# Performance work log

Hardware: AMD Instinct MI355X
Metric: run time of the kernel (lower is better)

## Reference

```python
import jax, jax.numpy as jnp
import numpy as np

# Scattering2D hyperparameters (kymatio-style Morlet filter bank)
J, L, M, N = 2, 8, 224, 224
SIGMA0 = 0.8
XI0 = 3.0 * np.pi / 4.0
SLANT = 4.0 / L


def _fold(h, k):
    """Fourier-domain subsampling / filter periodization: fold and average k x k blocks."""
    if k == 1:
        return h
    Mh, Nh = h.shape[-2], h.shape[-1]
    return h.reshape(h.shape[:-2] + (k, Mh // k, k, Nh // k)).mean(axis=(-4, -2))


def _freq_grid():
    wx = (2 * np.pi * np.fft.fftfreq(M)).astype(np.float64)[:, None]
    wy = (2 * np.pi * np.fft.fftfreq(N)).astype(np.float64)[None, :]
    return wx, wy


def _morlet_hat(theta, xi, sigma):
    wx, wy = _freq_grid()
    u = np.cos(theta) * wx + np.sin(theta) * wy
    v = -np.sin(theta) * wx + np.cos(theta) * wy
    gab = np.exp(-0.5 * sigma ** 2 * ((u - xi) ** 2 + (v / SLANT) ** 2))
    gauss = np.exp(-0.5 * sigma ** 2 * (u ** 2 + (v / SLANT) ** 2))
    kappa = np.exp(-0.5 * sigma ** 2 * xi ** 2)  # zero-mean Morlet correction
    return (gab - kappa * gauss).astype(np.float32)


def _build_filters():
    psi = {}
    for j in range(J):
        f = np.stack([_morlet_hat(l * np.pi / L, XI0 / 2 ** j, SIGMA0 * 2 ** j) for l in range(L)])
        psi[j] = [_fold(f, 2 ** r) for r in range(j + 1)]  # periodized to each resolution
    wx, wy = _freq_grid()
    sig_phi = SIGMA0 * 2 ** (J - 1)
    phi0 = np.exp(-0.5 * sig_phi ** 2 * (wx ** 2 + wy ** 2)).astype(np.float32)
    phi = [_fold(phi0, 2 ** r) for r in range(J)]
    return psi, phi


PSI, PHI = _build_filters()


def _scattering(x):
    # x: (B, C, M, N) float32 -> (B, C, K, M/2^J, N/2^J), K = 1 + J*L + L^2*J*(J-1)/2
    xh = jnp.fft.fft2(x)
    s0 = jnp.fft.ifft2(_fold(xh * PHI[0], 2 ** J)).real[..., None, :, :]
    s1s, s2s = [], []
    for j1 in range(J):
        # first order: bandpass, subsample to resolution j1, modulus
        u1h = _fold(xh[..., None, :, :] * PSI[j1][0], 2 ** j1)       # (B,C,L,M/2^j1,N/2^j1)
        u1 = jnp.abs(jnp.fft.ifft2(u1h))
        u1h2 = jnp.fft.fft2(u1)
        s1s.append(jnp.fft.ifft2(_fold(u1h2 * PHI[j1], 2 ** (J - j1))).real)
        for j2 in range(j1 + 1, J):
            # second order over all (theta1, theta2) pairs, vectorized over L x L
            u2h = _fold(u1h2[..., None, :, :] * PSI[j2][j1], 2 ** (j2 - j1))  # (B,C,L,L,.,.)
            u2 = jnp.abs(jnp.fft.ifft2(u2h))
            s2 = jnp.fft.ifft2(_fold(jnp.fft.fft2(u2) * PHI[j2], 2 ** (J - j2))).real
            s2s.append(s2.reshape(s2.shape[:2] + (L * L,) + s2.shape[-2:]))
    return jnp.concatenate([s0] + s1s + s2s, axis=2)


def setup_inputs() -> dict:
    key = jax.random.key(0)
    k1, k2, _ = jax.random.split(key, 3)
    x = jax.random.normal(k1, (16, 3, M, N), dtype=jnp.float32)
    W_last = jax.random.normal(k2, (1000, 243), dtype=jnp.float32) * 0.02
    b_last = jnp.zeros((1000,), dtype=jnp.float32)
    return {"x": x, "W_last": W_last, "b_last": b_last}


def reference(x, W_last, b_last):
    s = _scattering(x)                                   # (B, 3, 81, 56, 56)
    B = s.shape[0]
    s = s.reshape(B, s.shape[1] * s.shape[2], s.shape[3], s.shape[4])  # flatten(1,2)
    g = s.max(axis=(-2, -1))                             # global max pool -> (B, 243)
    return g @ W_last.T + b_last                         # (B, 1000)
```

## Files before the change

kernel.cpp:

```cpp
#include <hip/hip_runtime.h>
#include <math.h>

#define PI_D 3.14159265358979323846
#define PI_F 3.14159265358979323846f

#define IMG224 50176
#define IMG112 12544
static const size_t OFF_FT224F = 0;
static const size_t OFF_FT224I = 2048;
static const size_t OFF_FT112F = 4096;
static const size_t OFF_FT112I = 6144;
static const size_t OFF_PHW    = 8600;
static const size_t OFF_PSI   = 257152;
static const size_t OFF_GK    = 1122688;
static const size_t OFF_XH    = 1126784;
static const size_t OFF_POOL  = 5943680;

__device__ inline unsigned fkey(float v) {
    int b = __float_as_int(v);
    return (b >= 0) ? ((unsigned)b | 0x80000000u) : ~(unsigned)b;
}
__device__ inline float funkey(unsigned u) {
    int b = (u & 0x80000000u) ? (int)(u & 0x7fffffffu) : (int)~u;
    return __int_as_float(b);
}
__device__ inline void cmac(float2& a, float2 z, float2 w) {
    a.x += z.x * w.x - z.y * w.y;
    a.y += z.x * w.y + z.y * w.x;
}
__device__ inline float2 cmulc(float2 v, float c, float s) {
    return make_float2(v.x * c - v.y * s, v.x * s + v.y * c);
}

struct C7 { float s; float wr[3][3]; float wi[3][3]; };
__device__ inline void ld7(const float2* __restrict__ W7, C7& c) {
    c.s = W7[0].x;
#pragma unroll
    for (int m = 1; m <= 3; ++m)
#pragma unroll
        for (int k = 1; k <= 3; ++k) {
            float2 w = W7[m * 7 + k];
            c.wr[m - 1][k - 1] = w.x;
            c.wi[m - 1][k - 1] = w.y;
        }
}
__device__ inline void dft7(const C7& c, const float2 t[7], float2 X[7]) {
    float2 a1 = make_float2(t[1].x + t[6].x, t[1].y + t[6].y);
    float2 b1 = make_float2(t[1].x - t[6].x, t[1].y - t[6].y);
    float2 a2 = make_float2(t[2].x + t[5].x, t[2].y + t[5].y);
    float2 b2 = make_float2(t[2].x - t[5].x, t[2].y - t[5].y);
    float2 a3 = make_float2(t[3].x + t[4].x, t[3].y + t[4].y);
    float2 b3 = make_float2(t[3].x - t[4].x, t[3].y - t[4].y);
    float bx = c.s * t[0].x, by = c.s * t[0].y;
    X[0] = make_float2(c.s * (t[0].x + a1.x + a2.x + a3.x),
                       c.s * (t[0].y + a1.y + a2.y + a3.y));
#pragma unroll
    for (int k = 0; k < 3; ++k) {
        float Px = c.wr[0][k] * a1.x + c.wr[1][k] * a2.x + c.wr[2][k] * a3.x;
        float Py = c.wr[0][k] * a1.y + c.wr[1][k] * a2.y + c.wr[2][k] * a3.y;
        float Qx = c.wi[0][k] * b1.x + c.wi[1][k] * b2.x + c.wi[2][k] * b3.x;
        float Qy = c.wi[0][k] * b1.y + c.wi[1][k] * b2.y + c.wi[2][k] * b3.y;
        X[k + 1] = make_float2(bx + Px - Qy, by + Py + Qx);
        X[6 - k] = make_float2(bx + Px + Qy, by + Py - Qx);
    }
}

template<int SGN>
__device__ inline void fft16(float2* x) {
    const float C8  = 0.70710678118654752f;
    const float C16 = 0.92387953251128674f;
    const float S16 = 0.38268343236508977f;
    const float sg = (float)SGN;
    float2 g[16];
#pragma unroll
    for (int b = 0; b < 4; ++b) {
        float2 x0 = x[b], x1 = x[4 + b], x2 = x[8 + b], x3 = x[12 + b];
        float2 e0 = make_float2(x0.x + x2.x, x0.y + x2.y);
        float2 e1 = make_float2(x0.x - x2.x, x0.y - x2.y);
        float2 o0 = make_float2(x1.x + x3.x, x1.y + x3.y);
        float2 o1 = make_float2(x1.x - x3.x, x1.y - x3.y);
        float2 io1 = (SGN > 0) ? make_float2(-o1.y, o1.x) : make_float2(o1.y, -o1.x);
        g[b * 4 + 0] = make_float2(e0.x + o0.x, e0.y + o0.y);
        g[b * 4 + 2] = make_float2(e0.x - o0.x, e0.y - o0.y);
        g[b * 4 + 1] = make_float2(e1.x + io1.x, e1.y + io1.y);
        g[b * 4 + 3] = make_float2(e1.x - io1.x, e1.y - io1.y);
    }
    g[5]  = cmulc(g[5],  C16,  sg * S16);
    g[6]  = cmulc(g[6],  C8,   sg * C8);
    g[7]  = cmulc(g[7],  S16,  sg * C16);
    g[9]  = cmulc(g[9],  C8,   sg * C8);
    g[10] = (SGN > 0) ? make_float2(-g[10].y, g[10].x)
                      : make_float2(g[10].y, -g[10].x);
    g[11] = cmulc(g[11], -C8,  sg * C8);
    g[13] = cmulc(g[13], S16,  sg * C16);
    g[14] = cmulc(g[14], -C8,  sg * C8);
    g[15] = cmulc(g[15], -C16, -sg * S16);
#pragma unroll
    for (int p = 0; p < 4; ++p) {
        float2 x0 = g[p], x1 = g[4 + p], x2 = g[8 + p], x3 = g[12 + p];
        float2 e0 = make_float2(x0.x + x2.x, x0.y + x2.y);
        float2 e1 = make_float2(x0.x - x2.x, x0.y - x2.y);
        float2 o0 = make_float2(x1.x + x3.x, x1.y + x3.y);
        float2 o1 = make_float2(x1.x - x3.x, x1.y - x3.y);
        float2 io1 = (SGN > 0) ? make_float2(-o1.y, o1.x) : make_float2(o1.y, -o1.x);
        x[p + 0]  = make_float2(e0.x + o0.x, e0.y + o0.y);
        x[p + 8]  = make_float2(e0.x - o0.x, e0.y - o0.y);
        x[p + 4]  = make_float2(e1.x + io1.x, e1.y + io1.y);
        x[p + 12] = make_float2(e1.x - io1.x, e1.y - io1.y);
    }
}

__global__ void k_fact(float2* o, int N1, int N2, double sign, double scale, int r2) {
    int base3 = N1 * N1 + N2 * N2 + N2 * N1;
    int total = base3 + (r2 ? 63 : 0);
    int N = N1 * N2;
    for (int i = blockIdx.x * blockDim.x + threadIdx.x; i < total; i += blockDim.x * gridDim.x) {
        double ang; double sc = 1.0;
        if (i < N1 * N1) {
            int n1 = i / N1, k1 = i % N1;
            ang = sign * 2.0 * PI_D * (double)((n1 * k1) % N1) / (double)N1;
        } else if (i < N1 * N1 + N2 * N2) {
            int j = i - N1 * N1; int n2 = j / N2, k2 = j % N2;
            ang = sign * 2.0 * PI_D * (double)((n2 * k2) % N2) / (double)N2;
            sc = scale;
        } else if (i < base3) {
            int j = i - N1 * N1 - N2 * N2; int n2 = j / N1, k1 = j % N1;
            ang = sign * 2.0 * PI_D * (double)((n2 * k1) % N) / (double)N;
        } else if (i < base3 + 49) {
            int j = i - base3; int n = j / 7, k = j % 7;
            ang = sign * 2.0 * PI_D * (double)((n * k) % 7) / 7.0;
            sc = scale;
        } else {
            int k = i - base3 - 49;
            ang = sign * 2.0 * PI_D * (double)k / 14.0;
        }
        o[i] = make_float2((float)(sc * cos(ang)), (float)(sc * sin(ang)));
    }
}

__global__ void k_psi(float* out) {
    int i = blockIdx.x * blockDim.x + threadIdx.x;
    if (i >= 16 * IMG224) return;
    int jl = i / IMG224, p = i % IMG224;
    int r = p / 224, c = p % 224;
    int j = jl >> 3, l = jl & 7;
    float fr = (r < 112) ? (float)r : (float)(r - 224);
    float fc = (c < 112) ? (float)c : (float)(c - 224);
    float wx = 2.0f * PI_F * fr / 224.0f;
    float wy = 2.0f * PI_F * fc / 224.0f;
    float theta = (float)l * PI_F / 8.0f;
    float xi = (3.0f * PI_F / 4.0f) / (float)(1 << j);
    float sg = 0.8f * (float)(1 << j);
    float ct = cosf(theta), st = sinf(theta);
    float u = ct * wx + st * wy;
    float v = -st * wx + ct * wy;
    float vs = v * 2.0f;
    float s2 = 0.5f * sg * sg;
    float gab = expf(-s2 * ((u - xi) * (u - xi) + vs * vs));
    float gau = expf(-s2 * (u * u + vs * vs));
    float kap = expf(-s2 * xi * xi);
    out[i] = gab - kap * gau;
}

__global__ void k_zero(unsigned* gk, int n) {
    int i = blockIdx.x * blockDim.x + threadIdx.x;
    if (i < n) gk[i] = 0u;
}

template<int N1, int N2, int TA, int FOLD, int BS, int RMODE, int SGN>
__global__ __launch_bounds__(BS) void rk(
    const void* __restrict__ inBase, int inShift,
    const float* __restrict__ fltBase, int fltMask,
    const float2* __restrict__ FT, float2* __restrict__ out,
    int swzImg, int inStride, int inOff)
{
    constexpr int N = N1 * N2;
    constexpr int NIN = N * FOLD;
    constexpr int ZS = N + 2;
    constexpr int TS = N2 * (N1 + 1);
    constexpr int K1H = N1 / 2;
    constexpr int TAC = (RMODE == 2) ? TA / 2 : TA;
    __shared__ float2 Z[TA * ZS];
    __shared__ float2 T[TA * TS];
    const float2* TW = FT + N1 * N1 + N2 * N2;
    const int bx = blockIdx.x, a0 = blockIdx.y * TA, t = threadIdx.x;
    int gIn, gFlt, gOut;
    if (swzImg > 0) {
        int img = bx % swzImg, sub = bx / swzImg;
        gIn = img * inStride + inOff + (sub >> 3);
        gFlt = sub & fltMask;
        gOut = img * (gridDim.x / swzImg) + sub;
    } else if (swzImg < 0) {
        int lgF = -swzImg;
        int xcd = bx & 7, loc = bx >> 3;
        int img = xcd * ((int)gridDim.x >> (3 + lgF)) + (loc >> lgF);
        int f = loc & ((1 << lgF) - 1);
        gIn = img; gFlt = f & fltMask; gOut = (img << lgF) + f;
    } else {
        gIn = bx >> inShift; gFlt = bx & fltMask; gOut = bx;
    }

    if (RMODE == 1) {
        const float* in = (const float*)inBase + (size_t)gIn * N * N;
#pragma unroll
        for (int r = 0; r < TA; ++r)
            for (int b = t; b < N; b += BS)
                Z[r * ZS + b] = make_float2(in[(size_t)(a0 + r) * N + b], 0.f);
    } else if (RMODE == 2) {
        const float* in = (const float*)inBase + (size_t)gIn * N * N;
#pragma unroll
        for (int pr = 0; pr < TAC; ++pr)
            for (int b = t; b < N; b += BS) {
                size_t base = (size_t)(a0 + 2 * pr) * N + b;
                Z[pr * ZS + b] = make_float2(in[base], in[base + N]);
            }
    } else {
        const float2* in = (const float2*)inBase + (size_t)gIn * (NIN * NIN);
        const float* flt = fltBase + (size_t)gFlt * (NIN * NIN);
        const float s = 1.0f / (float)(FOLD * FOLD);
#pragma unroll
        for (int r = 0; r < TA; ++r) {
            int a = a0 + r;
            for (int b = t; b < N; b += BS) {
                float re = 0.f, im = 0.f;
#pragma unroll
                for (int i = 0; i < FOLD; ++i)
#pragma unroll
                    for (int j = 0; j < FOLD; ++j) {
                        int idx = (a + N * i) * NIN + (b + N * j);
                        float2 v = in[idx];
                        float f = flt[idx];
                        re += v.x * f; im += v.y * f;
                    }
                Z[r * ZS + b] = make_float2(re * s, im * s);
            }
        }
    }
    __syncthreads();
    for (int idx = t; idx < TAC * N2 * 2; idx += BS) {
        int r = idx / (N2 * 2);
        int rem = idx % (N2 * 2);
        int n2 = rem / 2, h = rem % 2;
        float2 xx[N1];
#pragma unroll
        for (int n1 = 0; n1 < N1; ++n1) xx[n1] = Z[r * ZS + n1 * N2 + n2];
        fft16<SGN>(xx);
#pragma unroll
        for (int kk = 0; kk < K1H; ++kk) {
            int k1 = h * K1H + kk;
            float2 tw = TW[n2 * N1 + k1];
            T[r * TS + n2 * (N1 + 1) + k1] = cmulc(xx[k1], tw.x, tw.y);
        }
    }
    __syncthreads();
    {
        const float2* W7  = FT + N1 * N1 + N2 * N2 + N2 * N1;
        const float2* T14 = W7 + 49;
        for (int idx = t; idx < TAC * N1; idx += BS) {
            int r = idx / N1, k1 = idx % N1;
            float2 E[7], O[7];
#pragma unroll
            for (int k = 0; k < 7; ++k) { E[k] = make_float2(0.f, 0.f); O[k] = make_float2(0.f, 0.f); }
            for (int m = 0; m < 7; ++m) {
                float2 te = T[r * TS + (2 * m) * (N1 + 1) + k1];
                float2 to = T[r * TS + (2 * m + 1) * (N1 + 1) + k1];
#pragma unroll
                for (int k = 0; k < 7; ++k) {
                    float2 w = W7[m * 7 + k];
                    cmac(E[k], te, w);
                    cmac(O[k], to, w);
                }
            }
#pragma unroll
            for (int k = 0; k < 14; ++k) {
                float2 tw = T14[k];
                float2 o_ = O[k % 7];
                float2 X = E[k % 7];
                X.x += o_.x * tw.x - o_.y * tw.y;
                X.y += o_.x * tw.y + o_.y * tw.x;
                Z[r * ZS + k1 + N1 * k] = X;
            }
        }
    }
    __syncthreads();
    if (RMODE == 2) {
#pragma unroll
        for (int pr = 0; pr < TAC; ++pr) {
            float2* oe = out + ((size_t)gOut * N + (a0 + 2 * pr)) * N;
            float2* oo = oe + N;
            for (int b = t; b < N; b += BS) {
                int mb = (b == 0) ? 0 : N - b;
                float2 zk = Z[pr * ZS + b];
                float2 zm = Z[pr * ZS + mb];
                oe[b] = make_float2(0.5f * (zk.x + zm.x), 0.5f * (zk.y - zm.y));
                oo[b] = make_float2(0.5f * (zk.y + zm.y), 0.5f * (zm.x - zk.x));
            }
        }
    } else {
#pragma unroll
        for (int r = 0; r < TA; ++r) {
            float2* o = out + ((size_t)gOut * N + (a0 + r)) * N;
            for (int b = t; b < N; b += BS) o[b] = Z[r * ZS + b];
        }
    }
}

template<int N1, int N2, int SPLIT, int BS, int SGN>
__global__ __launch_bounds__(BS) void ck1(
    const float2* __restrict__ in, const float2* __restrict__ FT, float2* __restrict__ out)
{
    constexpr int N = N1 * N2;
    constexpr int NC = N / SPLIT;
    const float2* TW = FT + N1 * N1 + N2 * N2;
    const int g = blockIdx.x / SPLIT, half = blockIdx.x % SPLIT;
    const int n2 = blockIdx.y, t = threadIdx.x;
    if (2 * t >= NC) return;
    const int b0 = 2 * t + half * NC;
    const float2* I = in + (size_t)g * N * N;
    float2 a0[16], a1[16];
#pragma unroll
    for (int n1 = 0; n1 < 16; ++n1) {
        float4 v = *reinterpret_cast<const float4*>(&I[(size_t)(n1 * N2 + n2) * N + b0]);
        a0[n1] = make_float2(v.x, v.y);
        a1[n1] = make_float2(v.z, v.w);
    }
    fft16<SGN>(a0);
    fft16<SGN>(a1);
#pragma unroll
    for (int k1 = 0; k1 < 16; ++k1) {
        float2 tw = TW[n2 * N1 + k1];
        float2 r0 = cmulc(a0[k1], tw.x, tw.y);
        float2 r1 = cmulc(a1[k1], tw.x, tw.y);
        *reinterpret_cast<float4*>(&out[((size_t)g * N + (k1 * N2 + n2)) * N + b0]) =
            make_float4(r0.x, r0.y, r1.x, r1.y);
    }
}

template<int N1, int N2, int SPLIT, int MODE, int BS>
__global__ __launch_bounds__(BS) void ck2(
    const float2* __restrict__ in, const float2* __restrict__ FT,
    float2* __restrict__ outc, float* __restrict__ outr)
{
    constexpr int N = N1 * N2;
    constexpr int NC = N / SPLIT;
    const int g = blockIdx.x / SPLIT, half = blockIdx.x % SPLIT;
    const int k1 = blockIdx.y, t = threadIdx.x;
    if (2 * t >= NC) return;
    const int b0 = 2 * t + half * NC;
    const float2* I = in + (size_t)g * N * N;
    const float2* W7  = FT + N1 * N1 + N2 * N2 + N2 * N1;
    const float2* T14 = W7 + 49;
    float2 E0[7], E1[7], O0[7], O1[7];
#pragma unroll
    for (int k = 0; k < 7; ++k) {
        E0[k] = make_float2(0.f, 0.f); E1[k] = make_float2(0.f, 0.f);
        O0[k] = make_float2(0.f, 0.f); O1[k] = make_float2(0.f, 0.f);
    }
#pragma unroll
    for (int m = 0; m < 7; ++m) {
        float4 ve = *reinterpret_cast<const float4*>(&I[(size_t)(k1 * 14 + 2 * m) * N + b0]);
        float4 vo = *reinterpret_cast<const float4*>(&I[(size_t)(k1 * 14 + 2 * m + 1) * N + b0]);
        float2 ve0 = make_float2(ve.x, ve.y), ve1 = make_float2(ve.z, ve.w);
        float2 vo0 = make_float2(vo.x, vo.y), vo1 = make_float2(vo.z, vo.w);
#pragma unroll
        for (int k = 0; k < 7; ++k) {
            float2 w = W7[m * 7 + k];
            cmac(E0[k], ve0, w); cmac(E1[k], ve1, w);
            cmac(O0[k], vo0, w); cmac(O1[k], vo1, w);
        }
    }
#pragma unroll
    for (int k = 0; k < 14; ++k) {
        float2 tw = T14[k];
        float2 r0 = E0[k % 7], r1 = E1[k % 7];
        float2 o0 = O0[k % 7], o1 = O1[k % 7];
        r0.x += o0.x * tw.x - o0.y * tw.y;
        r0.y += o0.x * tw.y + o0.y * tw.x;
        r1.x += o1.x * tw.x - o1.y * tw.y;
        r1.y += o1.x * tw.y + o1.y * tw.x;
        if (MODE == 0) {
            *reinterpret_cast<float4*>(&outc[((size_t)g * N + (k1 + N1 * k)) * N + b0]) =
                make_float4(r0.x, r0.y, r1.x, r1.y);
        } else {
            size_t o = ((size_t)g * N + (k1 + N1 * k)) * N + b0;
            outr[o]     = sqrtf(r0.x * r0.x + r0.y * r0.y);
            outr[o + 1] = sqrtf(r1.x * r1.x + r1.y * r1.y);
        }
    }
}

template<int SGN, int BS, int EPI>
__device__ inline void fft112_2d(float2* Z, const float2* __restrict__ FT, int t)
{
    constexpr int ZS = 113;
    constexpr int NCH = (112 * 16 + BS - 1) / BS;
    const float2* W2 = FT + 256;
    const float2* TW = FT + 256 + 49;
    C7 c7; ld7(W2, c7);
    for (int idx = t; idx < 112 * 7; idx += BS) {
        int r = idx % 112, n2 = idx / 112;
        float2 xx[16];
#pragma unroll
        for (int n1 = 0; n1 < 16; ++n1) xx[n1] = Z[r * ZS + n1 * 7 + n2];
        fft16<SGN>(xx);
#pragma unroll
        for (int k1 = 0; k1 < 16; ++k1) {
            float2 tw = TW[n2 * 16 + k1];
            Z[r * ZS + k1 * 7 + n2] = cmulc(xx[k1], tw.x, tw.y);
        }
    }
    __syncthreads();
    {
        float2 tv[NCH][7];
#pragma unroll
        for (int c = 0; c < NCH; ++c) {
            int idx = c * BS + t;
            if (idx < 112 * 16) {
                int r = idx >> 4, k1 = idx & 15;
#pragma unroll
                for (int m = 0; m < 7; ++m) tv[c][m] = Z[r * ZS + k1 * 7 + m];
            }
        }
        __syncthreads();
#pragma unroll
        for (int c = 0; c < NCH; ++c) {
            int idx = c * BS + t;
            if (idx < 112 * 16) {
                int r = idx >> 4, k1 = idx & 15;
                float2 X[7];
                dft7(c7, tv[c], X);
#pragma unroll
                for (int k = 0; k < 7; ++k) Z[r * ZS + k1 + 16 * k] = X[k];
            }
        }
    }
    __syncthreads();
    for (int idx = t; idx < 112 * 7; idx += BS) {
        int b = idx % 112, n2 = idx / 112;
        float2 xx[16];
#pragma unroll
        for (int n1 = 0; n1 < 16; ++n1) xx[n1] = Z[(n1 * 7 + n2) * ZS + b];
        fft16<SGN>(xx);
#pragma unroll
        for (int k1 = 0; k1 < 16; ++k1) {
            float2 tw = TW[n2 * 16 + k1];
            Z[(k1 * 7 + n2) * ZS + b] = cmulc(xx[k1], tw.x, tw.y);
        }
    }
    __syncthreads();
    {
        float2 tv[NCH][7];
#pragma unroll
        for (int c = 0; c < NCH; ++c) {
            int idx = c * BS + t;
            if (idx < 112 * 16) {
                int b = idx >> 4, k1 = idx & 15;
#pragma unroll
                for (int m = 0; m < 7; ++m) tv[c][m] = Z[(k1 * 7 + m) * ZS + b];
            }
        }
        __syncthreads();
#pragma unroll
        for (int c = 0; c < NCH; ++c) {
            int idx = c * BS + t;
            if (idx < 112 * 16) {
                int b = idx >> 4, k1 = idx & 15;
                float2 X[7];
                dft7(c7, tv[c], X);
#pragma unroll
                for (int k = 0; k < 7; ++k) {
                    Z[(k1 + 16 * k) * ZS + b] =
                        EPI ? make_float2(sqrtf(X[k].x * X[k].x + X[k].y * X[k].y), 0.f)
                            : X[k];
                }
            }
        }
    }
    __syncthreads();
}

template<int BS>
__global__ __launch_bounds__(BS) void sc2pipe(
    const float2* __restrict__ inBase, const float* __restrict__ psiBase,
    const float* __restrict__ taps, const float2* __restrict__ FTI,
    unsigned* __restrict__ gk, int slotBase, int inStride, int subShift)
{
    constexpr int ZS = 113;
    __shared__ float2 Z[112 * ZS];
    __shared__ float2 F[56 * 57];
    __shared__ float red[BS / 64];
    const int t = threadIdx.x, bx = blockIdx.x;
    const int nimg = (int)gridDim.x >> subShift;
    const int xcd = bx & 7, local = bx >> 3;
    const int img = xcd * (nimg >> 3) + (local >> subShift);
    const int sub = local & ((1 << subShift) - 1);
    const float2* in = inBase + (size_t)(img * inStride + (sub >> 3)) * (224 * 224);
    const float* flt = psiBase + (size_t)(sub & 7) * (224 * 224);
    float gw[6];
#pragma unroll
    for (int i = 0; i < 6; ++i) gw[i] = taps[i];

    for (int idx = t; idx < 112 * 112; idx += BS) {
        int a = idx / 112, b = idx % 112;
        float re = 0.f, im = 0.f;
#pragma unroll
        for (int i = 0; i < 2; ++i)
#pragma unroll
            for (int j = 0; j < 2; ++j) {
                int p = (a + 112 * i) * 224 + (b + 112 * j);
                float2 v = in[p]; float f = flt[p];
                re += v.x * f; im += v.y * f;
            }
        Z[a * ZS + b] = make_float2(re * 0.25f, im * 0.25f);
    }
    __syncthreads();

    fft112_2d<1, BS, 1>(Z, FTI, t);

    float* Ft = (float*)F;
    for (int idx = t; idx < 112 * 56; idx += BS) {
        int r = idx % 112, cp = idx / 112;
        int c0 = 2 * cp;
        float acc = gw[0] * Z[r * ZS + c0].x;
#pragma unroll
        for (int m = 1; m <= 5; ++m) {
            int cm = c0 - m; cm += (cm < 0) ? 112 : 0;
            int cq = c0 + m; cq -= (cq >= 112) ? 112 : 0;
            acc += gw[m] * (Z[r * ZS + cm].x + Z[r * ZS + cq].x);
        }
        Ft[r * 57 + cp] = acc;
    }
    __syncthreads();

    float mx = -INFINITY;
    for (int idx = t; idx < 56 * 56; idx += BS) {
        int j = idx % 56, ip = idx / 56;
        int r0 = 2 * ip;
        float acc = gw[0] * Ft[r0 * 57 + j];
#pragma unroll
        for (int m = 1; m <= 5; ++m) {
            int ra = r0 - m; ra += (ra < 0) ? 112 : 0;
            int rb = r0 + m; rb -= (rb >= 112) ? 112 : 0;
            acc += gw[m] * (Ft[ra * 57 + j] + Ft[rb * 57 + j]);
        }
        mx = fmaxf(mx, acc);
    }
    for (int off = 32; off > 0; off >>= 1) mx = fmaxf(mx, __shfl_down(mx, off, 64));
    if ((t & 63) == 0) red[t >> 6] = mx;
    __syncthreads();
    if (t == 0) {
#pragma unroll
        for (int w = 1; w < BS / 64; ++w) mx = fmaxf(mx, red[w]);
        atomicMax(&gk[img * 81 + slotBase + sub], fkey(mx));
    }
}

template<int SB, int BS>
__global__ __launch_bounds__(BS) void s1conv(
    const float* __restrict__ inBase, const float* __restrict__ taps,
    unsigned* __restrict__ gk, int slotBase, int slotShift, int slotMask)
{
    constexpr int OPB = 56 / SB;
    constexpr int IR  = 4 * OPB + 19;
    __shared__ float R2[IR][56];
    __shared__ float red[BS / 64];
    const int g = blockIdx.x, t = threadIdx.x;
    const int band = g % SB, grp = g / SB;
    const float* u = inBase + (size_t)grp * 50176;
    float gw[12];
#pragma unroll
    for (int i = 0; i < 12; ++i) gw[i] = taps[i];
    const int rbase = 4 * OPB * band - 11;
    for (int idx = t; idx < IR * 56; idx += BS) {
        int j = idx % 56, rr = idx / 56;
        int riw = rbase + rr;
        riw += (riw < 0) ? 224 : 0;
        riw -= (riw >= 224) ? 224 : 0;
        const float* row = u + riw * 224;
        int c0 = 4 * j;
        float acc = gw[0] * row[c0];
#pragma unroll
        for (int m = 1; m <= 11; ++m) {
            int cm = c0 - m; cm += (cm < 0) ? 224 : 0;
            int cq = c0 + m; cq -= (cq >= 224) ? 224 : 0;
            acc += gw[m] * (row[cm] + row[cq]);
        }
        R2[rr][j] = acc;
    }
    __syncthreads();
    float mx = -INFINITY;
    for (int idx = t; idx < OPB * 56; idx += BS) {
        int j = idx % 56, l = idx / 56;
        int base = 4 * l + 11;
        float acc = gw[0] * R2[base][j];
#pragma unroll
        for (int m = 1; m <= 11; ++m)
            acc += gw[m] * (R2[base - m][j] + R2[base + m][j]);
        mx = fmaxf(mx, acc);
    }
    for (int off = 32; off > 0; off >>= 1) mx = fmaxf(mx, __shfl_down(mx, off, 64));
    if ((t & 63) == 0) red[t >> 6] = mx;
    __syncthreads();
    if (t == 0) {
#pragma unroll
        for (int w = 1; w < BS / 64; ++w) mx = fmaxf(mx, red[w]);
        int slot = slotBase + ((grp >> slotShift) * 81) + (grp & slotMask);
        atomicMax(&gk[slot], fkey(mx));
    }
}

__global__ void k_linear(const unsigned* __restrict__ gk, const float* __restrict__ Wl,
                         const float* __restrict__ bl, float* __restrict__ out)
{
    int i = blockIdx.x * blockDim.x + threadIdx.x;
    if (i >= 16 * 1000) return;
    int b = i / 1000, o = i % 1000;
    float s = bl[o];
    for (int f = 0; f < 243; ++f)
        s += funkey(gk[b * 243 + f]) * Wl[o * 243 + f];
    out[i] = s;
}

static float g_taps[32];
static bool g_taps_init = false;
static void host_taps() {
    if (g_taps_init) return;
    const double s2 = 0.5 * 1.6 * 1.6;
    for (int m = 0; m < 16; ++m) {
        double acc = 0.0;
        for (int k = 0; k < 112; ++k) {
            double w0 = 2.0 * PI_D * (double)k / 224.0;
            double w1 = 2.0 * PI_D * (double)(k - 112) / 224.0;
            double F = 0.5 * (exp(-s2 * w0 * w0) + exp(-s2 * w1 * w1));
            acc += F * cos(2.0 * PI_D * (double)k * (double)m / 112.0);
        }
        g_taps[m] = (float)(acc / 112.0);
    }
    for (int m = 0; m < 16; ++m) {
        double acc = 0.0;
        for (int k = 0; k < 224; ++k) {
            double fr = (k < 112) ? (double)k : (double)(k - 224);
            double w = 2.0 * PI_D * fr / 224.0;
            acc += exp(-s2 * w * w) * cos(2.0 * PI_D * (double)k * (double)m / 224.0);
        }
        g_taps[16 + m] = (float)(acc / 224.0);
    }
    g_taps_init = true;
}

extern "C" void kernel_launch(void* const* d_in, const int* in_sizes, int n_in,
                              void* d_out, int out_size, void* d_ws, size_t ws_size,
                              hipStream_t stream)
{
    const float* x  = (const float*)d_in[0];
    const float* Wl = (const float*)d_in[1];
    const float* bl = (const float*)d_in[2];
    float* out = (float*)d_out;
    float* ws = (float*)d_ws;

    float2* FT224F = (float2*)(ws + OFF_FT224F);
    float2* FT224I = (float2*)(ws + OFF_FT224I);
    float2* FT112I = (float2*)(ws + OFF_FT112I);
    float* TAPS = ws + OFF_PHW;
    float* PSI0 = ws + OFF_PSI;
    float* PSI1 = ws + OFF_PSI + 8 * IMG224;
    unsigned* GK = (unsigned*)(ws + OFF_GK);
    float2* XH  = (float2*)(ws + OFF_XH);
    float* A0  = ws + OFF_POOL;
    float* A1  = A0 + 19267584;
    float* A23 = A1 + 19267584;

    host_taps();
    hipMemcpyAsync(TAPS, g_taps, 32 * sizeof(float), hipMemcpyHostToDevice, stream);
    k_fact<<<4, 256, 0, stream>>>(FT224F, 16, 14, -1.0, 1.0, 1);
    k_fact<<<4, 256, 0, stream>>>(FT224I, 16, 14,  1.0, 1.0 / 224.0, 1);
    k_fact<<<1, 256, 0, stream>>>(FT112I, 16, 7,   1.0, 1.0 / 112.0, 0);
    k_psi<<<(16 * IMG224 + 255) / 256, 256, 0, stream>>>(ws + OFF_PSI);
    k_zero<<<(3888 + 255) / 256, 256, 0, stream>>>(GK, 3888);

    rk<16, 14, 4, 1, 128, 2, -1><<<dim3(48, 56), 128, 0, stream>>>(x, 0, nullptr, 0, FT224F, (float2*)A0, 0, 0, 0);
    ck1<16, 14, 2, 64, -1><<<dim3(96, 14), 64, 0, stream>>>((float2*)A0, FT224F, (float2*)A1);
    ck2<16, 14, 2, 0, 64><<<dim3(96, 16), 64, 0, stream>>>((float2*)A1, FT224F, XH, nullptr);

    s1conv<8, 256><<<48 * 8, 256, 0, stream>>>(x, TAPS + 16, GK, 0, 0, 0);

    sc2pipe<1024><<<384, 1024, 0, stream>>>(XH, PSI1, TAPS, FT112I, GK, 9, 1, 3);

    for (int c2 = 0; c2 < 2; ++c2) {
        rk<16, 14, 4, 1, 128, 0, 1><<<dim3(192, 56), 128, 0, stream>>>(
            XH, 1, PSI0 + (size_t)(4 * c2) * IMG224, 3, FT224I, (float2*)A0, -2, 0, 0);
        ck1<16, 14, 2, 64, 1><<<dim3(384, 14), 64, 0, stream>>>((float2*)A0, FT224I, (float2*)A1);
        ck2<16, 14, 2, 1, 64><<<dim3(384, 16), 64, 0, stream>>>((float2*)A1, FT224I, nullptr, A23);
        s1conv<8, 256><<<192 * 8, 256, 0, stream>>>(A23, TAPS + 16, GK, 1 + 4 * c2, 2, 3);
        rk<16, 14, 4, 1, 128, 2, -1><<<dim3(192, 56), 128, 0, stream>>>(A23, 0, nullptr, 0, FT224F, (float2*)A0, 0, 0, 0);
        ck1<16, 14, 2, 64, -1><<<dim3(384, 14), 64, 0, stream>>>((float2*)A0, FT224F, (float2*)A1);
        ck2<16, 14, 2, 0, 64><<<dim3(384, 16), 64, 0, stream>>>((float2*)A1, FT224F, (float2*)A0, nullptr);
        sc2pipe<1024><<<1536, 1024, 0, stream>>>((float2*)A0, PSI1, TAPS, FT112I, GK, 17 + 32 * c2, 4, 5);
    }

    k_linear<<<(16000 + 255) / 256, 256, 0, stream>>>(GK, Wl, bl, out);
}
```

Measured before the change: 917.2 us.

## Replace j=1 wavelet FFT pipeline with truncated 9x9 spatial convolution

The second-level wavelet stage, which did a forward 224 FFT, a Fourier-domain multiply with fold, and a 112 inverse FFT per channel, becomes a direct strided 9x9 complex spatial convolution. The taps are precomputed on the host by an inverse DFT of the psi_1 filter truncated to 9x9. Modulus, lowpass and max-pool are fused in the same kernel, and the forward FFT of the first-order output is dropped along with the j=1 psi filter generation. This removes the large FFT passes and their global-memory traffic, but truncating the filter support to 9x9 is an approximation that may reduce accuracy.

```diff
diff --git a/kernel.cpp b/kernel.cpp
--- a/kernel.cpp
+++ b/kernel.cpp
@@ -5,11 +5,8 @@
 #define PI_F 3.14159265358979323846f
 
 #define IMG224 50176
-#define IMG112 12544
 static const size_t OFF_FT224F = 0;
 static const size_t OFF_FT224I = 2048;
-static const size_t OFF_FT112F = 4096;
-static const size_t OFF_FT112I = 6144;
 static const size_t OFF_PHW    = 8600;
 static const size_t OFF_PSI   = 257152;
 static const size_t OFF_GK    = 1122688;
@@ -30,39 +27,6 @@
 }
 __device__ inline float2 cmulc(float2 v, float c, float s) {
     return make_float2(v.x * c - v.y * s, v.x * s + v.y * c);
-}
-
-struct C7 { float s; float wr[3][3]; float wi[3][3]; };
-__device__ inline void ld7(const float2* __restrict__ W7, C7& c) {
-    c.s = W7[0].x;
-#pragma unroll
-    for (int m = 1; m <= 3; ++m)
-#pragma unroll
-        for (int k = 1; k <= 3; ++k) {
-            float2 w = W7[m * 7 + k];
-            c.wr[m - 1][k - 1] = w.x;
-            c.wi[m - 1][k - 1] = w.y;
-        }
-}
-__device__ inline void dft7(const C7& c, const float2 t[7], float2 X[7]) {
-    float2 a1 = make_float2(t[1].x + t[6].x, t[1].y + t[6].y);
-    float2 b1 = make_float2(t[1].x - t[6].x, t[1].y - t[6].y);
-    float2 a2 = make_float2(t[2].x + t[5].x, t[2].y + t[5].y);
-    float2 b2 = make_float2(t[2].x - t[5].x, t[2].y - t[5].y);
-    float2 a3 = make_float2(t[3].x + t[4].x, t[3].y + t[4].y);
-    float2 b3 = make_float2(t[3].x - t[4].x, t[3].y - t[4].y);
-    float bx = c.s * t[0].x, by = c.s * t[0].y;
-    X[0] = make_float2(c.s * (t[0].x + a1.x + a2.x + a3.x),
-                       c.s * (t[0].y + a1.y + a2.y + a3.y));
-#pragma unroll
-    for (int k = 0; k < 3; ++k) {
-        float Px = c.wr[0][k] * a1.x + c.wr[1][k] * a2.x + c.wr[2][k] * a3.x;
-        float Py = c.wr[0][k] * a1.y + c.wr[1][k] * a2.y + c.wr[2][k] * a3.y;
-        float Qx = c.wi[0][k] * b1.x + c.wi[1][k] * b2.x + c.wi[2][k] * b3.x;
-        float Qy = c.wi[0][k] * b1.y + c.wi[1][k] * b2.y + c.wi[2][k] * b3.y;
-        X[k + 1] = make_float2(bx + Px - Qy, by + Py + Qx);
-        X[6 - k] = make_float2(bx + Px + Qy, by + Py - Qx);
-    }
 }
 
 template<int SGN>
@@ -140,17 +104,16 @@
 
 __global__ void k_psi(float* out) {
     int i = blockIdx.x * blockDim.x + threadIdx.x;
-    if (i >= 16 * IMG224) return;
-    int jl = i / IMG224, p = i % IMG224;
+    if (i >= 8 * IMG224) return;
+    int l = i / IMG224, p = i % IMG224;
     int r = p / 224, c = p % 224;
-    int j = jl >> 3, l = jl & 7;
     float fr = (r < 112) ? (float)r : (float)(r - 224);
     float fc = (c < 112) ? (float)c : (float)(c - 224);
     float wx = 2.0f * PI_F * fr / 224.0f;
     float wy = 2.0f * PI_F * fc / 224.0f;
     float theta = (float)l * PI_F / 8.0f;
-    float xi = (3.0f * PI_F / 4.0f) / (float)(1 << j);
-    float sg = 0.8f * (float)(1 << j);
+    float xi = 3.0f * PI_F / 4.0f;
+    float sg = 0.8f;
     float ct = cosf(theta), st = sinf(theta);
     float u = ct * wx + st * wy;
     float v = -st * wx + ct * wy;
@@ -389,169 +352,94 @@
     }
 }
 
-template<int SGN, int BS, int EPI>
-__device__ inline void fft112_2d(float2* Z, const float2* __restrict__ FT, int t)
+template<int BA, int BS>
+__global__ __launch_bounds__(BS) void sc2conv(
+    const float* __restrict__ uBase, const float2* __restrict__ gpsiG,
+    const float* __restrict__ taps, unsigned* __restrict__ gk,
+    int slotBase, int ps)
 {
-    constexpr int ZS = 113;
-    constexpr int NCH = (112 * 16 + BS - 1) / BS;
-    const float2* W2 = FT + 256;
-    const float2* TW = FT + 256 + 49;
-    C7 c7; ld7(W2, c7);
-    for (int idx = t; idx < 112 * 7; idx += BS) {
-        int r = idx % 112, n2 = idx / 112;
-        float2 xx[16];
-#pragma unroll
-        for (int n1 = 0; n1 < 16; ++n1) xx[n1] = Z[r * ZS + n1 * 7 + n2];
-        fft16<SGN>(xx);
-#pragma unroll
-        for (int k1 = 0; k1 < 16; ++k1) {
-            float2 tw = TW[n2 * 16 + k1];
-            Z[r * ZS + k1 * 7 + n2] = cmulc(xx[k1], tw.x, tw.y);
-        }
-    }
-    __syncthreads();
-    {
-        float2 tv[NCH][7];
-#pragma unroll
-        for (int c = 0; c < NCH; ++c) {
-            int idx = c * BS + t;
-            if (idx < 112 * 16) {
-                int r = idx >> 4, k1 = idx & 15;
-#pragma unroll
-                for (int m = 0; m < 7; ++m) tv[c][m] = Z[r * ZS + k1 * 7 + m];
-            }
-        }
-        __syncthreads();
-#pragma unroll
-        for (int c = 0; c < NCH; ++c) {
-            int idx = c * BS + t;
-            if (idx < 112 * 16) {
-                int r = idx >> 4, k1 = idx & 15;
-                float2 X[7];
-                dft7(c7, tv[c], X);
-#pragma unroll
-                for (int k = 0; k < 7; ++k) Z[r * ZS + k1 + 16 * k] = X[k];
-            }
-        }
-    }
-    __syncthreads();
-    for (int idx = t; idx < 112 * 7; idx += BS) {
-        int b = idx % 112, n2 = idx / 112;
-        float2 xx[16];
-#pragma unroll
-        for (int n1 = 0; n1 < 16; ++n1) xx[n1] = Z[(n1 * 7 + n2) * ZS + b];
-        fft16<SGN>(xx);
-#pragma unroll
-        for (int k1 = 0; k1 < 16; ++k1) {
-            float2 tw = TW[n2 * 16 + k1];
-            Z[(k1 * 7 + n2) * ZS + b] = cmulc(xx[k1], tw.x, tw.y);
-        }
-    }
-    __syncthreads();
-    {
-        float2 tv[NCH][7];
-#pragma unroll
-        for (int c = 0; c < NCH; ++c) {
-            int idx = c * BS + t;
-            if (idx < 112 * 16) {
-                int b = idx >> 4, k1 = idx & 15;
-#pragma unroll
-                for (int m = 0; m < 7; ++m) tv[c][m] = Z[(k1 * 7 + m) * ZS + b];
-            }
-        }
-        __syncthreads();
-#pragma unroll
-        for (int c = 0; c < NCH; ++c) {
-            int idx = c * BS + t;
-            if (idx < 112 * 16) {
-                int b = idx >> 4, k1 = idx & 15;
-                float2 X[7];
-                dft7(c7, tv[c], X);
-#pragma unroll
-                for (int k = 0; k < 7; ++k) {
-                    Z[(k1 + 16 * k) * ZS + b] =
-                        EPI ? make_float2(sqrtf(X[k].x * X[k].x + X[k].y * X[k].y), 0.f)
-                            : X[k];
-                }
-            }
-        }
-    }
-    __syncthreads();
-}
-
-template<int BS>
-__global__ __launch_bounds__(BS) void sc2pipe(
-    const float2* __restrict__ inBase, const float* __restrict__ psiBase,
-    const float* __restrict__ taps, const float2* __restrict__ FTI,
-    unsigned* __restrict__ gk, int slotBase, int inStride, int subShift)
-{
-    constexpr int ZS = 113;
-    __shared__ float2 Z[112 * ZS];
-    __shared__ float2 F[56 * 57];
+    constexpr int NB = 56 / BA;
+    constexpr int UR = 4 * BA + 25;
+    constexpr int UW = 232;
+    constexpr int VR = 2 * BA + 9;
+    __shared__ float U[UR * UW];
+    __shared__ float V[VR * 112];
+    __shared__ float B1[VR * 56];
+    __shared__ float2 GT[8 * 81];
     __shared__ float red[BS / 64];
     const int t = threadIdx.x, bx = blockIdx.x;
-    const int nimg = (int)gridDim.x >> subShift;
-    const int xcd = bx & 7, local = bx >> 3;
-    const int img = xcd * (nimg >> 3) + (local >> subShift);
-    const int sub = local & ((1 << subShift) - 1);
-    const float2* in = inBase + (size_t)(img * inStride + (sub >> 3)) * (224 * 224);
-    const float* flt = psiBase + (size_t)(sub & 7) * (224 * 224);
+    const int p = bx / NB, band = bx % NB;
+    const int a0 = band * BA;
+    const int img = p >> ps, sub = p & ((1 << ps) - 1);
+    const float* u = uBase + (size_t)p * 50176;
     float gw[6];
 #pragma unroll
     for (int i = 0; i < 6; ++i) gw[i] = taps[i];
-
-    for (int idx = t; idx < 112 * 112; idx += BS) {
-        int a = idx / 112, b = idx % 112;
-        float re = 0.f, im = 0.f;
-#pragma unroll
-        for (int i = 0; i < 2; ++i)
-#pragma unroll
-            for (int j = 0; j < 2; ++j) {
-                int p = (a + 112 * i) * 224 + (b + 112 * j);
-                float2 v = in[p]; float f = flt[p];
-                re += v.x * f; im += v.y * f;
-            }
-        Z[a * ZS + b] = make_float2(re * 0.25f, im * 0.25f);
+    for (int i = t; i < 8 * 81; i += BS) GT[i] = gpsiG[i];
+    const int r0 = 4 * a0 - 14;
+    for (int idx = t; idx < UR * UW; idx += BS) {
+        int rr = idx / UW, cc = idx % UW;
+        int gr = r0 + rr;
+        gr += (gr < 0) ? 224 : 0;
+        gr -= (gr >= 224) ? 224 : 0;
+        int gc = cc - 4;
+        gc += (gc < 0) ? 224 : 0;
+        gc -= (gc >= 224) ? 224 : 0;
+        U[idx] = u[gr * 224 + gc];
     }
     __syncthreads();
 
-    fft112_2d<1, BS, 1>(Z, FTI, t);
-
-    float* Ft = (float*)F;
-    for (int idx = t; idx < 112 * 56; idx += BS) {
-        int r = idx % 112, cp = idx / 112;
-        int c0 = 2 * cp;
-        float acc = gw[0] * Z[r * ZS + c0].x;
-#pragma unroll
-        for (int m = 1; m <= 5; ++m) {
-            int cm = c0 - m; cm += (cm < 0) ? 112 : 0;
-            int cq = c0 + m; cq -= (cq >= 112) ? 112 : 0;
-            acc += gw[m] * (Z[r * ZS + cm].x + Z[r * ZS + cq].x);
-        }
-        Ft[r * 57 + cp] = acc;
-    }
-    __syncthreads();
-
-    float mx = -INFINITY;
-    for (int idx = t; idx < 56 * 56; idx += BS) {
-        int j = idx % 56, ip = idx / 56;
-        int r0 = 2 * ip;
-        float acc = gw[0] * Ft[r0 * 57 + j];
-#pragma unroll
-        for (int m = 1; m <= 5; ++m) {
-            int ra = r0 - m; ra += (ra < 0) ? 112 : 0;
-            int rb = r0 + m; rb -= (rb >= 112) ? 112 : 0;
-            acc += gw[m] * (Ft[ra * 57 + j] + Ft[rb * 57 + j]);
-        }
-        mx = fmaxf(mx, acc);
-    }
-    for (int off = 32; off > 0; off >>= 1) mx = fmaxf(mx, __shfl_down(mx, off, 64));
-    if ((t & 63) == 0) red[t >> 6] = mx;
-    __syncthreads();
-    if (t == 0) {
-#pragma unroll
-        for (int w = 1; w < BS / 64; ++w) mx = fmaxf(mx, red[w]);
-        atomicMax(&gk[img * 81 + slotBase + sub], fkey(mx));
+    for (int l2 = 0; l2 < 8; ++l2) {
+        const float2* G = GT + l2 * 81;
+        for (int idx = t; idx < VR * 112; idx += BS) {
+            int ri = idx / 112, j = idx % 112;
+            float re = 0.f, im = 0.f;
+#pragma unroll
+            for (int m = -4; m <= 4; ++m) {
+                const float* urow = U + (2 * ri + 4 - m) * UW + 2 * j;
+#pragma unroll
+                for (int n = -4; n <= 4; ++n) {
+                    float2 g = G[(m + 4) * 9 + (n + 4)];
+                    float uv = urow[4 - n];
+                    re += uv * g.x; im += uv * g.y;
+                }
+            }
+            V[idx] = sqrtf(re * re + im * im);
+        }
+        __syncthreads();
+        for (int idx = t; idx < VR * 56; idx += BS) {
+            int ri = idx / 56, b = idx % 56;
+            int c0 = 2 * b;
+            const float* vr = V + ri * 112;
+            float acc = gw[0] * vr[c0];
+#pragma unroll
+            for (int m = 1; m <= 5; ++m) {
+                int cm = c0 - m; cm += (cm < 0) ? 112 : 0;
+                int cq = c0 + m; cq -= (cq >= 112) ? 112 : 0;
+                acc += gw[m] * (vr[cm] + vr[cq]);
+            }
+            B1[idx] = acc;
+        }
+        __syncthreads();
+        float mx = -INFINITY;
+        for (int idx = t; idx < BA * 56; idx += BS) {
+            int la = idx / 56, b = idx % 56;
+            int base = 2 * la + 5;
+            float acc = gw[0] * B1[base * 56 + b];
+#pragma unroll
+            for (int m = 1; m <= 5; ++m)
+                acc += gw[m] * (B1[(base - m) * 56 + b] + B1[(base + m) * 56 + b]);
+            mx = fmaxf(mx, acc);
+        }
+        for (int off = 32; off > 0; off >>= 1) mx = fmaxf(mx, __shfl_down(mx, off, 64));
+        if ((t & 63) == 0) red[t >> 6] = mx;
+        __syncthreads();
+        if (t == 0) {
+#pragma unroll
+            for (int w = 1; w < BS / 64; ++w) mx = fmaxf(mx, red[w]);
+            atomicMax(&gk[img * 81 + slotBase + (sub << 3) + l2], fkey(mx));
+        }
+        __syncthreads();
     }
 }
 
@@ -621,31 +509,72 @@
     out[i] = s;
 }
 
-static float g_taps[32];
-static bool g_taps_init = false;
-static void host_taps() {
-    if (g_taps_init) return;
-    const double s2 = 0.5 * 1.6 * 1.6;
+static float g_all[32 + 8 * 81 * 2];
+static bool g_tab_init = false;
+static void host_tables() {
+    if (g_tab_init) return;
+    const double s2p = 0.5 * 1.6 * 1.6;
     for (int m = 0; m < 16; ++m) {
         double acc = 0.0;
         for (int k = 0; k < 112; ++k) {
             double w0 = 2.0 * PI_D * (double)k / 224.0;
             double w1 = 2.0 * PI_D * (double)(k - 112) / 224.0;
-            double F = 0.5 * (exp(-s2 * w0 * w0) + exp(-s2 * w1 * w1));
+            double F = 0.5 * (exp(-s2p * w0 * w0) + exp(-s2p * w1 * w1));
             acc += F * cos(2.0 * PI_D * (double)k * (double)m / 112.0);
         }
-        g_taps[m] = (float)(acc / 112.0);
+        g_all[m] = (float)(acc / 112.0);
     }
     for (int m = 0; m < 16; ++m) {
         double acc = 0.0;
         for (int k = 0; k < 224; ++k) {
             double fr = (k < 112) ? (double)k : (double)(k - 224);
             double w = 2.0 * PI_D * fr / 224.0;
-            acc += exp(-s2 * w * w) * cos(2.0 * PI_D * (double)k * (double)m / 224.0);
-        }
-        g_taps[16 + m] = (float)(acc / 224.0);
-    }
-    g_taps_init = true;
+            acc += exp(-s2p * w * w) * cos(2.0 * PI_D * (double)k * (double)m / 224.0);
+        }
+        g_all[16 + m] = (float)(acc / 224.0);
+    }
+    static double innRe[224][9], innIm[224][9];
+    const double xi = (3.0 * PI_D / 4.0) / 2.0, sg = 1.6;
+    const double s2 = 0.5 * sg * sg;
+    const double kap = exp(-s2 * xi * xi);
+    for (int l = 0; l < 8; ++l) {
+        double th = (double)l * PI_D / 8.0;
+        double ct = cos(th), st = sin(th);
+        for (int kr = 0; kr < 224; ++kr)
+            for (int n = 0; n < 9; ++n) { innRe[kr][n] = 0.0; innIm[kr][n] = 0.0; }
+        for (int kr = 0; kr < 224; ++kr) {
+            double fr = (kr < 112) ? (double)kr : (double)(kr - 224);
+            double wx = 2.0 * PI_D * fr / 224.0;
+            for (int kc = 0; kc < 224; ++kc) {
+                double fc = (kc < 112) ? (double)kc : (double)(kc - 224);
+                double wy = 2.0 * PI_D * fc / 224.0;
+                double uu = ct * wx + st * wy;
+                double vv = -st * wx + ct * wy;
+                double vs = vv / 0.5;
+                double val = exp(-s2 * ((uu - xi) * (uu - xi) + vs * vs))
+                           - kap * exp(-s2 * (uu * uu + vs * vs));
+                for (int n = 0; n < 9; ++n) {
+                    double ang = 2.0 * PI_D * fc * (double)(n - 4) / 224.0;
+                    innRe[kr][n] += val * cos(ang);
+                    innIm[kr][n] += val * sin(ang);
+                }
+            }
+        }
+        for (int m = 0; m < 9; ++m)
+            for (int n = 0; n < 9; ++n) {
+                double re = 0.0, im = 0.0;
+                for (int kr = 0; kr < 224; ++kr) {
+                    double fr = (kr < 112) ? (double)kr : (double)(kr - 224);
+                    double ang = 2.0 * PI_D * fr * (double)(m - 4) / 224.0;
+                    double c = cos(ang), s = sin(ang);
+                    re += innRe[kr][n] * c - innIm[kr][n] * s;
+                    im += innRe[kr][n] * s + innIm[kr][n] * c;
+                }
+                g_all[32 + 2 * (l * 81 + m * 9 + n)]     = (float)(re / 50176.0);
+                g_all[32 + 2 * (l * 81 + m * 9 + n) + 1] = (float)(im / 50176.0);
+            }
+    }
+    g_tab_init = true;
 }
 
 extern "C" void kernel_launch(void* const* d_in, const int* in_sizes, int n_in,
@@ -660,22 +589,20 @@
 
     float2* FT224F = (float2*)(ws + OFF_FT224F);
     float2* FT224I = (float2*)(ws + OFF_FT224I);
-    float2* FT112I = (float2*)(ws + OFF_FT112I);
     float* TAPS = ws + OFF_PHW;
+    float2* GPSI = (float2*)(ws + OFF_PHW + 32);
     float* PSI0 = ws + OFF_PSI;
-    float* PSI1 = ws + OFF_PSI + 8 * IMG224;
     unsigned* GK = (unsigned*)(ws + OFF_GK);
     float2* XH  = (float2*)(ws + OFF_XH);
     float* A0  = ws + OFF_POOL;
     float* A1  = A0 + 19267584;
     float* A23 = A1 + 19267584;
 
-    host_taps();
-    hipMemcpyAsync(TAPS, g_taps, 32 * sizeof(float), hipMemcpyHostToDevice, stream);
+    host_tables();
+    hipMemcpyAsync(TAPS, g_all, sizeof(g_all), hipMemcpyHostToDevice, stream);
     k_fact<<<4, 256, 0, stream>>>(FT224F, 16, 14, -1.0, 1.0, 1);
     k_fact<<<4, 256, 0, stream>>>(FT224I, 16, 14,  1.0, 1.0 / 224.0, 1);
-    k_fact<<<1, 256, 0, stream>>>(FT112I, 16, 7,   1.0, 1.0 / 112.0, 0);
-    k_psi<<<(16 * IMG224 + 255) / 256, 256, 0, stream>>>(ws + OFF_PSI);
+    k_psi<<<(8 * IMG224 + 255) / 256, 256, 0, stream>>>(PSI0);
     k_zero<<<(3888 + 255) / 256, 256, 0, stream>>>(GK, 3888);
 
     rk<16, 14, 4, 1, 128, 2, -1><<<dim3(48, 56), 128, 0, stream>>>(x, 0, nullptr, 0, FT224F, (float2*)A0, 0, 0, 0);
@@ -684,7 +611,7 @@
 
     s1conv<8, 256><<<48 * 8, 256, 0, stream>>>(x, TAPS + 16, GK, 0, 0, 0);
 
-    sc2pipe<1024><<<384, 1024, 0, stream>>>(XH, PSI1, TAPS, FT112I, GK, 9, 1, 3);
+    sc2conv<8, 256><<<48 * 7, 256, 0, stream>>>(x, GPSI, TAPS, GK, 9, 0);
 
     for (int c2 = 0; c2 < 2; ++c2) {
         rk<16, 14, 4, 1, 128, 0, 1><<<dim3(192, 56), 128, 0, stream>>>(
@@ -692,10 +619,7 @@
         ck1<16, 14, 2, 64, 1><<<dim3(384, 14), 64, 0, stream>>>((float2*)A0, FT224I, (float2*)A1);
         ck2<16, 14, 2, 1, 64><<<dim3(384, 16), 64, 0, stream>>>((float2*)A1, FT224I, nullptr, A23);
         s1conv<8, 256><<<192 * 8, 256, 0, stream>>>(A23, TAPS + 16, GK, 1 + 4 * c2, 2, 3);
-        rk<16, 14, 4, 1, 128, 2, -1><<<dim3(192, 56), 128, 0, stream>>>(A23, 0, nullptr, 0, FT224F, (float2*)A0, 0, 0, 0);
-        ck1<16, 14, 2, 64, -1><<<dim3(384, 14), 64, 0, stream>>>((float2*)A0, FT224F, (float2*)A1);
-        ck2<16, 14, 2, 0, 64><<<dim3(384, 16), 64, 0, stream>>>((float2*)A1, FT224F, (float2*)A0, nullptr);
-        sc2pipe<1024><<<1536, 1024, 0, stream>>>((float2*)A0, PSI1, TAPS, FT112I, GK, 17 + 32 * c2, 4, 5);
+        sc2conv<8, 256><<<192 * 7, 256, 0, stream>>>(A23, GPSI, TAPS, GK, 17 + 32 * c2, 2);
     }
 
     k_linear<<<(16000 + 255) / 256, 256, 0, stream>>>(GK, Wl, bl, out);
```

After: 1.138 ms. 1.24x slower.
